# Kernel optimization log

Measured on AMD Instinct MI355X. Metric: run time of the kernel, lower is better.

## Reference

```python
import jax, jax.numpy as jnp
import numpy as np

EPS = 1e-5

def conv3x3(x, w, b):
    # x: [B,C,H,W], w: [O,I,3,3], padding=1 (SAME)
    y = jax.lax.conv_general_dilated(x, w, window_strides=(1, 1),
                                     padding=[(1, 1), (1, 1)],
                                     dimension_numbers=('NCHW', 'OIHW', 'NCHW'))
    return y + b[None, :, None, None]

def pool_block(x, k):
    # exact adaptive avg pool: 300 is divisible by the output size, block size k
    B, C, H, W = x.shape
    return x.reshape(B, C, H // k, k, W // k, k).mean(axis=(3, 5))

def upsample_nearest(x, k):
    # equivalent to the nested python-loop slice-assign in RIA
    return jnp.repeat(jnp.repeat(x, k, axis=2), k, axis=3)

def _conv_param(key, o, i):
    k1, k2 = jax.random.split(key)
    fan_in = i * 9
    w = jax.random.normal(k1, (o, i, 3, 3), jnp.float32) * np.sqrt(2.0 / fan_in)
    b = jax.random.normal(k2, (o,), jnp.float32) * 0.01
    return w, b

def setup_inputs() -> dict:
    key = jax.random.key(0)
    ks = jax.random.split(key, 16)
    inp = {}
    inp['im'] = jax.random.normal(ks[0], (32, 3, 300, 300), jnp.float32)
    inp['w1'], inp['b1'] = _conv_param(ks[1], 8, 3)
    inp['w2'], inp['b2'] = _conv_param(ks[2], 16, 8)
    inp['w3'], inp['b3'] = _conv_param(ks[3], 32, 16)
    inp['w4'], inp['b4'] = _conv_param(ks[4], 16, 32)
    inp['w5'], inp['b5'] = _conv_param(ks[5], 8, 16)
    inp['wc5'], inp['bc5'] = _conv_param(ks[6], 8, 16)
    inp['wc10'], inp['bc10'] = _conv_param(ks[7], 8, 16)
    inp['wc15'], inp['bc15'] = _conv_param(ks[8], 8, 16)
    inp['wg'], inp['bg'] = _conv_param(ks[9], 8, 24)
    inp['wm'], inp['bm'] = _conv_param(ks[10], 8, 24)
    inp['bn_w'] = jnp.ones((8,), jnp.float32)
    inp['bn_b'] = jnp.zeros((8,), jnp.float32)
    inp['w11'], inp['b11'] = _conv_param(ks[11], 1, 8)
    inp['gamma'] = jnp.full((1,), 0.3, jnp.float32)
    return inp

def reference(im, w1, b1, w2, b2, w3, b3, w4, b4, w5, b5,
              wc5, bc5, wc10, bc10, wc15, bc15,
              wg, bg, wm, bm, bn_w, bn_b, w11, b11, gamma):
    # attention conv chain 3->8->16->32->16->8
    x = conv3x3(im, w1, b1)
    x = conv3x3(x, w2, b2)
    x = conv3x3(x, w3, b3)
    x = conv3x3(x, w4, b4)
    x = conv3x3(x, w5, b5)  # [B,8,300,300]

    # RIA: triple-scale pooled context, nearest-upsampled and fused
    up5 = upsample_nearest(pool_block(x, 5), 5)
    up10 = upsample_nearest(pool_block(x, 10), 10)
    up15 = upsample_nearest(pool_block(x, 15), 15)
    c5 = conv3x3(jnp.concatenate([x, up5], axis=1), wc5, bc5)
    c10 = conv3x3(jnp.concatenate([x, up10], axis=1), wc10, bc10)
    c15 = conv3x3(jnp.concatenate([x, up15], axis=1), wc15, bc15)
    g_in = jnp.concatenate([c5, c10, c15], axis=1)  # [B,24,300,300]

    # gated conv (activation=None): conv(x) * sigmoid(mask_conv(x)), then BN (batch stats)
    gated = conv3x3(g_in, wg, bg) * jax.nn.sigmoid(conv3x3(g_in, wm, bm))
    mean = gated.mean(axis=(0, 2, 3), keepdims=True)
    var = gated.var(axis=(0, 2, 3), keepdims=True)
    gated = (gated - mean) * jax.lax.rsqrt(var + EPS)
    gated = gated * bn_w[None, :, None, None] + bn_b[None, :, None, None]

    # 8->1 conv, sigmoid attention map, residual gating with gamma
    att = jax.nn.sigmoid(conv3x3(gated, w11, b11))  # [B,1,300,300]
    out = gamma * (att * im) + (1.0 - gamma) * im
    return out
```

## Files before the change

kernel.cpp:

```cpp
#include <hip/hip_runtime.h>
#include <hip/hip_bf16.h>
#include <math.h>

typedef __hip_bfloat16 bf16;
typedef __attribute__((ext_vector_type(8))) __bf16 bf16x8;
typedef __attribute__((ext_vector_type(8))) unsigned short u16x8;
typedef __attribute__((ext_vector_type(4))) float f32x4;

#define H_ 300
#define W_ 300
#define HW_ 90000
#define NBATCH 32
#define RB 512

__device__ __forceinline__ float b2f(unsigned short u) {
    return __uint_as_float((unsigned int)u << 16);
}
__device__ __forceinline__ unsigned short f2u(float v) {
    bf16 b = __float2bfloat16(v);
    return *reinterpret_cast<unsigned short*>(&b);
}
__device__ __forceinline__ float sigm(float x) { return 1.f / (1.f + __expf(-x)); }
__device__ __forceinline__ unsigned int packbf(float a, float b) {
    return (unsigned int)f2u(a) | ((unsigned int)f2u(b) << 16);
}

__global__ void pack_all_k(
    const float* __restrict__ w1, const float* __restrict__ w2,
    const float* __restrict__ w3, const float* __restrict__ w4,
    const float* __restrict__ w5, const float* __restrict__ wc5,
    const float* __restrict__ wc10, const float* __restrict__ wc15,
    const float* __restrict__ wg, const float* __restrict__ wm,
    unsigned short* __restrict__ WP)
{
    const float *a = nullptr, *bsec = nullptr;
    int cs = 999, CO = 0, CI = 0, CP = 8, NS = 3, NG = 1, off = 0, special = 0;
    switch (blockIdx.x) {
        case 0: a = w2;  CO = 16; CI = 8;  CP = 8;  NS = 3; off = 0;     break;
        case 1: a = w3;  CO = 32; CI = 16; CP = 16; NS = 5; NG = 2; off = 2048;  break;
        case 2: a = w4;  CO = 16; CI = 32; CP = 32; NS = 9; off = 8192;  break;
        case 3: a = w5;  CO = 8;  CI = 16; CP = 16; NS = 5; off = 13312; break;
        case 4: special = 1; CO = 32; CI = 32; CP = 32; NS = 9; NG = 2;
                off = 16384; break;
        case 5: a = wg; bsec = wm; cs = 8; CO = 16; CI = 24; CP = 32; NS = 9;
                off = 25600; break;
        case 6: a = w1;  CO = 8;  CI = 3;  CP = 8;  NS = 3; off = 30720; break;
    }
    unsigned short* outp = WP + off;
    int TPK = 32 / CP;
    int total = NS * NG * 512;
    for (int idx = threadIdx.x; idx < total; idx += 256) {
        int j = idx & 7;
        int lane = (idx >> 3) & 63;
        int g = (idx >> 9) % NG;
        int s = idx / (512 * NG);
        int col = lane & 15, kg = lane >> 4;
        int kk = kg * 8 + j;
        int tt = kk / CP, ci = kk % CP;
        int tap = s * TPK + tt;
        float v = 0.f;
        if (special) {
            int o = ci >> 3, c8 = ci & 7;
            int convid = (g == 0) ? (col < 8 ? 0 : 1) : (col < 8 ? 2 : -1);
            if (tap < 9 && convid >= 0) {
                const float* wc = (convid == 0) ? wc5 : (convid == 1) ? wc10 : wc15;
                int colc = col & 7;
                if (o == 0) v = wc[(colc * 16 + c8) * 9 + tap];
                else if (o == convid + 1) v = wc[(colc * 16 + 8 + c8) * 9 + tap];
            }
        } else {
            int co = g * 16 + col;
            if (tap < 9 && ci < CI && co < CO)
                v = (co >= cs) ? bsec[((co - cs) * CI + ci) * 9 + tap]
                               : a[(co * CI + ci) * 9 + tap];
        }
        outp[idx] = f2u(v);
    }
}

template <int CIN, int CINP, int COUT, int NGI, int MODE, int TH>
__global__ __launch_bounds__(256) void mfconv_k(
    const unsigned short* __restrict__ src,
    const unsigned short* __restrict__ wpack,
    const float* __restrict__ bias0, const float* __restrict__ bias1,
    unsigned short* __restrict__ out, int co_total, int co_off)
{
    constexpr int TPK = 32 / CINP;
    constexpr int NSTEP = (9 + TPK - 1) / TPK;
    constexpr int OCT = CINP / 8;
    constexpr int NPX = (TH + 2) * 34;

    __shared__ __align__(16) unsigned short s_in[OCT * NPX * 8];

    int b = blockIdx.z;
    int x0 = blockIdx.x * 32, y0 = blockIdx.y * TH;
    int tid = threadIdx.x;
    int lane = tid & 63, wv = tid >> 6;
    bool interior = (x0 >= 1) && (x0 + 32 < W_) && (y0 >= 1) && (y0 + TH < H_);

    if (MODE == 3) {
        const float* sf = reinterpret_cast<const float*>(src) + (size_t)b * 3 * HW_;
        if (interior) {
            const float* sf0 = sf + (size_t)(y0 - 1) * W_ + (x0 - 1);
            for (int e = tid; e < NPX; e += 256) {
                int y = e / 34;
                size_t o = (size_t)e + (size_t)y * 266;
                u16x8 v = {0, 0, 0, 0, 0, 0, 0, 0};
                v[0] = f2u(sf0[o]);
                v[1] = f2u(sf0[HW_ + o]);
                v[2] = f2u(sf0[2 * HW_ + o]);
                *(u16x8*)&s_in[e * 8] = v;
            }
        } else {
            for (int e = tid; e < NPX; e += 256) {
                int y = e / 34, x = e - y * 34;
                int gy = y0 + y - 1, gx = x0 + x - 1;
                u16x8 v = {0, 0, 0, 0, 0, 0, 0, 0};
                if (gy >= 0 && gy < H_ && gx >= 0 && gx < W_) {
                    size_t o = (size_t)gy * W_ + gx;
                    v[0] = f2u(sf[o]);
                    v[1] = f2u(sf[HW_ + o]);
                    v[2] = f2u(sf[2 * HW_ + o]);
                }
                *(u16x8*)&s_in[e * 8] = v;
            }
        }
    } else {
        const unsigned short* sb = src + (size_t)b * CIN * HW_;
        int oct = (OCT == 1) ? 0 : (wv % OCT);
        int phase = (OCT == 4) ? 0 : (wv / OCT);
        if (interior) {
            const unsigned short* sb0 =
                sb + ((size_t)(y0 - 1) * W_ + (x0 - 1)) * CIN + oct * 8;
            for (int px = lane + phase * 64; px < NPX; px += 256 / OCT) {
                int y = px / 34;
                u16x8 v;
                if (CIN == CINP || oct * 8 < CIN)
                    v = *(const u16x8*)&sb0[(size_t)(px + y * 266) * CIN];
                else
                    v = (u16x8){0, 0, 0, 0, 0, 0, 0, 0};
                *(u16x8*)&s_in[(oct * NPX + px) * 8] = v;
            }
        } else {
            for (int px = lane + phase * 64; px < NPX; px += 256 / OCT) {
                int y = px / 34, x = px - y * 34;
                int gy = y0 + y - 1, gx = x0 + x - 1;
                u16x8 v = {0, 0, 0, 0, 0, 0, 0, 0};
                if (gy >= 0 && gy < H_ && gx >= 0 && gx < W_ &&
                    (CIN == CINP || oct * 8 < CIN))
                    v = *(const u16x8*)&sb[((size_t)gy * W_ + gx) * CIN + oct * 8];
                *(u16x8*)&s_in[(oct * NPX + px) * 8] = v;
            }
        }
    }

    bf16x8 bw[NGI][NSTEP];
#pragma unroll
    for (int gi = 0; gi < NGI; ++gi)
#pragma unroll
        for (int s = 0; s < NSTEP; ++s)
            bw[gi][s] = *(const bf16x8*)&wpack[((s * NGI + gi) * 64 + lane) * 8];

    int col = lane & 15, kg = lane >> 4;

    float bias_r[NGI][4];
#pragma unroll
    for (int gi = 0; gi < NGI; ++gi)
#pragma unroll
        for (int r = 0; r < 4; ++r) {
            if (MODE == 2)
                bias_r[0][r] = (kg < 2) ? bias0[kg * 4 + r] : bias1[(kg - 2) * 4 + r];
            else {
                int co_l = gi * 16 + kg * 4 + r;
                bias_r[gi][r] = (co_l < COUT) ? bias0[co_l] : 0.f;
            }
        }

    __syncthreads();

    if constexpr (OCT == 4) {
        int myb = wv * (TH / 4);
#pragma unroll
        for (int tx = 0; tx < 2; ++tx) {
            int pbase = kg * NPX + tx * 16 + col;
            bf16x8 fr[3][3];
#pragma unroll
            for (int r = 0; r < 2; ++r)
#pragma unroll
                for (int dx = 0; dx < 3; ++dx)
                    fr[r][dx] =
                        *(const bf16x8*)&s_in[(pbase + (myb + r) * 34 + dx) * 8];
#pragma unroll
            for (int ii = 0; ii < TH / 4; ++ii) {
#pragma unroll
                for (int dx = 0; dx < 3; ++dx)
                    fr[(ii + 2) % 3][dx] =
                        *(const bf16x8*)&s_in[(pbase + (myb + ii + 2) * 34 + dx) * 8];

                f32x4 acc[NGI];
#pragma unroll
                for (int gi = 0; gi < NGI; ++gi) acc[gi] = {0.f, 0.f, 0.f, 0.f};
#pragma unroll
                for (int dy = 0; dy < 3; ++dy)
#pragma unroll
                    for (int dx = 0; dx < 3; ++dx) {
                        bf16x8 a = fr[(ii + dy) % 3][dx];
#pragma unroll
                        for (int gi = 0; gi < NGI; ++gi)
                            acc[gi] = __builtin_amdgcn_mfma_f32_16x16x32_bf16(
                                bw[gi][dy * 3 + dx], a, acc[gi], 0, 0, 0);
                    }

                int gy = y0 + myb + ii;
                int gxx = x0 + tx * 16 + col;
                if (gy < H_) {
                    if (MODE == 2) {
                        float v0 = acc[0].x + bias_r[0][0];
                        float v1 = acc[0].y + bias_r[0][1];
                        float v2 = acc[0].z + bias_r[0][2];
                        float v3 = acc[0].w + bias_r[0][3];
                        float m0 = __shfl_xor(v0, 32), m1 = __shfl_xor(v1, 32);
                        float m2 = __shfl_xor(v2, 32), m3 = __shfl_xor(v3, 32);
                        if (kg < 2 && gxx < W_) {
                            uint2 st;
                            st.x = packbf(v0 * sigm(m0), v1 * sigm(m1));
                            st.y = packbf(v2 * sigm(m2), v3 * sigm(m3));
                            *(uint2*)&out[(((size_t)b * HW_ + (size_t)gy * W_ +
                                            gxx) * 8) + kg * 4] = st;
                        }
                    } else {
#pragma unroll
                        for (int gi = 0; gi < NGI; ++gi) {
                            int co_g = gi * 16 + kg * 4;
                            if (co_g < COUT && gxx < W_) {
                                uint2 st;
                                st.x = packbf(acc[gi].x + bias_r[gi][0],
                                              acc[gi].y + bias_r[gi][1]);
                                st.y = packbf(acc[gi].z + bias_r[gi][2],
                                              acc[gi].w + bias_r[gi][3]);
                                *(uint2*)&out[((size_t)b * HW_ +
                                               (size_t)gy * W_ + gxx) *
                                                  co_total + co_off + co_g] = st;
                            }
                        }
                    }
                }
            }
        }
    } else {
        int offs[NSTEP];
#pragma unroll
        for (int s = 0; s < NSTEP; ++s) {
            int t = s * TPK + kg / OCT;
            if (t > 8) t = 8;
            offs[s] = ((t / 3) * 34 + (t % 3)) * 8 + (kg % OCT) * (NPX * 8);
        }

#pragma unroll
        for (int i = 0; i < TH / 2; ++i) {
            int m = wv * (TH / 2) + i;
            int my = m >> 1, tx = m & 1;
            int gy = y0 + my;
            if (gy >= H_) continue;
            int base = (my * 34 + tx * 16 + col) * 8;

            f32x4 acc[NGI];
#pragma unroll
            for (int gi = 0; gi < NGI; ++gi) acc[gi] = {0.f, 0.f, 0.f, 0.f};
#pragma unroll
            for (int s = 0; s < NSTEP; ++s) {
                bf16x8 a = *(const bf16x8*)&s_in[base + offs[s]];
#pragma unroll
                for (int gi = 0; gi < NGI; ++gi)
                    acc[gi] = __builtin_amdgcn_mfma_f32_16x16x32_bf16(
                        bw[gi][s], a, acc[gi], 0, 0, 0);
            }

            int gxx = x0 + tx * 16 + col;
#pragma unroll
            for (int gi = 0; gi < NGI; ++gi) {
                int co_g = gi * 16 + kg * 4;
                if (co_g < COUT && gxx < W_) {
                    uint2 st;
                    st.x = packbf(acc[gi].x + bias_r[gi][0],
                                  acc[gi].y + bias_r[gi][1]);
                    st.y = packbf(acc[gi].z + bias_r[gi][2],
                                  acc[gi].w + bias_r[gi][3]);
                    *(uint2*)&out[((size_t)b * HW_ + (size_t)gy * W_ + gxx) *
                                      co_total + co_off + co_g] = st;
                }
            }
        }
    }
}

__global__ __launch_bounds__(256) void convc3_k(
    const unsigned short* __restrict__ src,
    const unsigned short* __restrict__ p5, const unsigned short* __restrict__ p10,
    const unsigned short* __restrict__ p15,
    const unsigned short* __restrict__ wpack,
    const float* __restrict__ bc5, const float* __restrict__ bc10,
    const float* __restrict__ bc15, unsigned short* __restrict__ out)
{
    constexpr int TH = 16;
    constexpr int NPX = (TH + 2) * 34;
    __shared__ __align__(16) unsigned short s_in[4 * NPX * 8];

    int b = blockIdx.z;
    int x0 = blockIdx.x * 32, y0 = blockIdx.y * TH;
    int tid = threadIdx.x;
    int lane = tid & 63, wv = tid >> 6;
    bool interior = (x0 >= 1) && (x0 + 32 < W_) && (y0 >= 1) && (y0 + TH < H_);

    const unsigned short* sb = src + (size_t)b * 8 * HW_;
    const unsigned short* pb5 = p5 + (size_t)b * 8 * 3600;
    const unsigned short* pb10 = p10 + (size_t)b * 8 * 900;
    const unsigned short* pb15 = p15 + (size_t)b * 8 * 400;

    int oct = wv;
    if (interior) {
        const unsigned short* sb0 = sb + ((size_t)(y0 - 1) * W_ + (x0 - 1)) * 8;
        for (int px = lane; px < NPX; px += 64) {
            int y = px / 34;
            u16x8 v;
            if (oct == 0) {
                v = *(const u16x8*)&sb0[(size_t)(px + y * 266) * 8];
            } else {
                int x = px - y * 34;
                int gy = y0 - 1 + y, gx = x0 - 1 + x;
                const unsigned short* pp =
                    (oct == 1) ? &pb5[((size_t)(gy / 5) * 60 + gx / 5) * 8]
                    : (oct == 2) ? &pb10[((size_t)(gy / 10) * 30 + gx / 10) * 8]
                                 : &pb15[((size_t)(gy / 15) * 20 + gx / 15) * 8];
                v = *(const u16x8*)pp;
            }
            *(u16x8*)&s_in[(oct * NPX + px) * 8] = v;
        }
    } else {
        for (int px = lane; px < NPX; px += 64) {
            int y = px / 34, x = px - y * 34;
            int gy = y0 + y - 1, gx = x0 + x - 1;
            u16x8 v = {0, 0, 0, 0, 0, 0, 0, 0};
            if (gy >= 0 && gy < H_ && gx >= 0 && gx < W_) {
                if (oct == 0)
                    v = *(const u16x8*)&sb[((size_t)gy * W_ + gx) * 8];
                else if (oct == 1)
                    v = *(const u16x8*)&pb5[((size_t)(gy / 5) * 60 + gx / 5) * 8];
                else if (oct == 2)
                    v = *(const u16x8*)&pb10[((size_t)(gy / 10) * 30 + gx / 10) * 8];
                else
                    v = *(const u16x8*)&pb15[((size_t)(gy / 15) * 20 + gx / 15) * 8];
            }
            *(u16x8*)&s_in[(oct * NPX + px) * 8] = v;
        }
    }

    bf16x8 bw[2][9];
#pragma unroll
    for (int g = 0; g < 2; ++g)
#pragma unroll
        for (int s = 0; s < 9; ++s)
            bw[g][s] = *(const bf16x8*)&wpack[((s * 2 + g) * 64 + lane) * 8];

    int col = lane & 15, kg = lane >> 4;
    float bias_r[2][4];
#pragma unroll
    for (int r = 0; r < 4; ++r) {
        bias_r[0][r] = (kg < 2) ? bc5[kg * 4 + r] : bc10[(kg - 2) * 4 + r];
        bias_r[1][r] = (kg < 2) ? bc15[kg * 4 + r] : 0.f;
    }

    __syncthreads();

    int myb = wv * (TH / 4);
#pragma unroll
    for (int tx = 0; tx < 2; ++tx) {
        int pbase = kg * NPX + tx * 16 + col;
        bf16x8 fr[3][3];
#pragma unroll
        for (int r = 0; r < 2; ++r)
#pragma unroll
            for (int dx = 0; dx < 3; ++dx)
                fr[r][dx] = *(const bf16x8*)&s_in[(pbase + (myb + r) * 34 + dx) * 8];
#pragma unroll
        for (int ii = 0; ii < TH / 4; ++ii) {
#pragma unroll
            for (int dx = 0; dx < 3; ++dx)
                fr[(ii + 2) % 3][dx] =
                    *(const bf16x8*)&s_in[(pbase + (myb + ii + 2) * 34 + dx) * 8];

            f32x4 acc[2];
            acc[0] = {0.f, 0.f, 0.f, 0.f};
            acc[1] = {0.f, 0.f, 0.f, 0.f};
#pragma unroll
            for (int dy = 0; dy < 3; ++dy)
#pragma unroll
                for (int dx = 0; dx < 3; ++dx) {
                    bf16x8 a = fr[(ii + dy) % 3][dx];
                    acc[0] = __builtin_amdgcn_mfma_f32_16x16x32_bf16(
                        bw[0][dy * 3 + dx], a, acc[0], 0, 0, 0);
                    acc[1] = __builtin_amdgcn_mfma_f32_16x16x32_bf16(
                        bw[1][dy * 3 + dx], a, acc[1], 0, 0, 0);
                }

            int gy = y0 + myb + ii;
            int gxx = x0 + tx * 16 + col;
            if (gy < H_ && gxx < W_) {
                size_t pxo = ((size_t)b * HW_ + (size_t)gy * W_ + gxx) * 24;
                uint2 st0;
                st0.x = packbf(acc[0].x + bias_r[0][0], acc[0].y + bias_r[0][1]);
                st0.y = packbf(acc[0].z + bias_r[0][2], acc[0].w + bias_r[0][3]);
                *(uint2*)&out[pxo + kg * 4] = st0;
                if (kg < 2) {
                    uint2 st1;
                    st1.x = packbf(acc[1].x + bias_r[1][0], acc[1].y + bias_r[1][1]);
                    st1.y = packbf(acc[1].z + bias_r[1][2], acc[1].w + bias_r[1][3]);
                    *(uint2*)&out[pxo + 16 + kg * 4] = st1;
                }
            }
        }
    }
}

__global__ __launch_bounds__(256) void pool5_k(const unsigned short* __restrict__ x,
                                               unsigned short* __restrict__ p5,
                                               int n)
{
    int idx = blockIdx.x * 256 + threadIdx.x;
    if (idx >= n) return;
    int b = idx / 3600;
    int rem = idx - b * 3600;
    int i = rem / 60, j = rem - i * 60;
    const unsigned short* src =
        x + ((size_t)b * HW_ + (size_t)(i * 5) * W_ + j * 5) * 8;
    float ss[8] = {0, 0, 0, 0, 0, 0, 0, 0};
#pragma unroll
    for (int r = 0; r < 5; ++r)
#pragma unroll
        for (int c = 0; c < 5; ++c) {
            u16x8 v = *(const u16x8*)&src[((size_t)r * W_ + c) * 8];
#pragma unroll
            for (int k = 0; k < 8; ++k) ss[k] += b2f(v[k]);
        }
    uint4 st;
    st.x = packbf(ss[0] * 0.04f, ss[1] * 0.04f);
    st.y = packbf(ss[2] * 0.04f, ss[3] * 0.04f);
    st.z = packbf(ss[4] * 0.04f, ss[5] * 0.04f);
    st.w = packbf(ss[6] * 0.04f, ss[7] * 0.04f);
    *(uint4*)&p5[(size_t)idx * 8] = st;
}

template <int R, int OD>
__device__ __forceinline__ void poolr_body(const unsigned short* __restrict__ p5,
                                           unsigned short* __restrict__ po, int idx)
{
    int b = idx / (OD * OD);
    int rem = idx - b * OD * OD;
    int i = rem / OD, j = rem - i * OD;
    const unsigned short* src =
        p5 + ((size_t)b * 3600 + (size_t)(i * R) * 60 + j * R) * 8;
    float ss[8] = {0, 0, 0, 0, 0, 0, 0, 0};
    const float inv = 1.f / (R * R);
#pragma unroll
    for (int r = 0; r < R; ++r)
#pragma unroll
        for (int c = 0; c < R; ++c) {
            u16x8 v = *(const u16x8*)&src[((size_t)r * 60 + c) * 8];
#pragma unroll
            for (int k = 0; k < 8; ++k) ss[k] += b2f(v[k]);
        }
    uint4 st;
    st.x = packbf(ss[0] * inv, ss[1] * inv);
    st.y = packbf(ss[2] * inv, ss[3] * inv);
    st.z = packbf(ss[4] * inv, ss[5] * inv);
    st.w = packbf(ss[6] * inv, ss[7] * inv);
    *(uint4*)&po[(size_t)idx * 8] = st;
}

__global__ __launch_bounds__(256) void poolrs_k(const unsigned short* __restrict__ p5,
                                                unsigned short* __restrict__ p10,
                                                unsigned short* __restrict__ p15,
                                                int n10, int n15)
{
    int idx = blockIdx.x * 256 + threadIdx.x;
    if (idx < n10) {
        poolr_body<2, 30>(p5, p10, idx);
    } else {
        idx -= n10;
        if (idx < n15) poolr_body<3, 20>(p5, p15, idx);
    }
}

__global__ __launch_bounds__(256) void reduce_k(
    const unsigned short* __restrict__ gated, float2* __restrict__ partials)
{
    int bx = blockIdx.x;
    int tid = threadIdx.x;
    float s[8] = {0, 0, 0, 0, 0, 0, 0, 0};
    float s2[8] = {0, 0, 0, 0, 0, 0, 0, 0};
    const size_t N = (size_t)NBATCH * HW_;
    for (size_t i = (size_t)bx * 256 + tid; i < N; i += (size_t)RB * 256) {
        u16x8 v = *(const u16x8*)&gated[i * 8];
#pragma unroll
        for (int k = 0; k < 8; ++k) {
            float f = b2f(v[k]);
            s[k] += f;
            s2[k] += f * f;
        }
    }
#pragma unroll
    for (int off = 32; off > 0; off >>= 1) {
#pragma unroll
        for (int k = 0; k < 8; ++k) {
            s[k] += __shfl_down(s[k], off);
            s2[k] += __shfl_down(s2[k], off);
        }
    }
    __shared__ float2 red[4][8];
    int lane = tid & 63, wvi = tid >> 6;
    if (lane == 0) {
#pragma unroll
        for (int k = 0; k < 8; ++k) red[wvi][k] = make_float2(s[k], s2[k]);
    }
    __syncthreads();
    if (tid < 8) {
        float a = 0.f, b2 = 0.f;
        for (int i = 0; i < 4; ++i) { a += red[i][tid].x; b2 += red[i][tid].y; }
        partials[tid * RB + bx] = make_float2(a, b2);
    }
}

__global__ __launch_bounds__(256) void stats_fold_k(
    const float2* __restrict__ partials, const float* __restrict__ bn_w,
    const float* __restrict__ bn_b, const float* __restrict__ w11,
    const float* __restrict__ b11, float* __restrict__ wfold)
{
    __shared__ float sc[8], tc[8];
    __shared__ float2 acc8[8];
    int tid = threadIdx.x;
    int c = tid >> 5, sl = tid & 31;
    float s = 0.f, s2 = 0.f;
    for (int i = sl; i < RB; i += 32) {
        float2 p = partials[c * RB + i];
        s += p.x;
        s2 += p.y;
    }
#pragma unroll
    for (int off = 16; off > 0; off >>= 1) {
        s += __shfl_down(s, off, 32);
        s2 += __shfl_down(s2, off, 32);
    }
    if (sl == 0) acc8[c] = make_float2(s, s2);
    __syncthreads();
    if (tid < 8) {
        double ds = acc8[tid].x, ds2 = acc8[tid].y;
        double N = (double)NBATCH * HW_;
        double mean = ds / N;
        double var = ds2 / N - mean * mean;
        float rstd = (float)(1.0 / sqrt(var + 1e-5));
        float scv = bn_w[tid] * rstd;
        sc[tid] = scv;
        tc[tid] = bn_b[tid] - (float)mean * scv;
    }
    __syncthreads();
    if (tid < 72) {
        int t = tid >> 3, ci = tid & 7;
        wfold[tid] = w11[ci * 9 + t] * sc[ci];
    }
    if (tid == 72) {
        float a = b11[0];
        for (int i = 0; i < 72; ++i) a += w11[i] * tc[i / 9];
        wfold[72] = a;
    }
}

__global__ __launch_bounds__(256) void final_k(
    const unsigned short* __restrict__ gated, const float* __restrict__ wf,
    const float* __restrict__ im, const float* __restrict__ gamma,
    float* __restrict__ out)
{
    __shared__ __align__(16) unsigned short s_g[1156 * 8];
    __shared__ float s_w[80];

    int b = blockIdx.z;
    int x0 = blockIdx.x * 32, y0 = blockIdx.y * 32;
    int tid = threadIdx.x;
    bool interior = (x0 >= 1) && (x0 + 32 < W_) && (y0 >= 1) && (y0 + 32 < H_);

    if (tid < 73) s_w[tid] = wf[tid];

    const unsigned short* gb = gated + (size_t)b * HW_ * 8;
    if (interior) {
        const unsigned short* gb0 = gb + ((size_t)(y0 - 1) * W_ + (x0 - 1)) * 8;
        for (int e = tid; e < 1156; e += 256) {
            int y = e / 34;
            u16x8 v = *(const u16x8*)&gb0[(size_t)(e + y * 266) * 8];
            *(u16x8*)&s_g[e * 8] = v;
        }
    } else {
        for (int e = tid; e < 1156; e += 256) {
            int y = e / 34, x = e - y * 34;
            int gy = y0 + y - 1, gx = x0 + x - 1;
            u16x8 v = {0, 0, 0, 0, 0, 0, 0, 0};
            if (gy >= 0 && gy < H_ && gx >= 0 && gx < W_)
                v = *(const u16x8*)&gb[((size_t)gy * W_ + gx) * 8];
            *(u16x8*)&s_g[e * 8] = v;
        }
    }
    __syncthreads();

    int qx = (tid & 15) * 2, qy = (tid >> 4) * 2;
    float f[4];
    float gm = *gamma;
#pragma unroll
    for (int p = 0; p < 4; ++p) {
        int ly = qy + (p >> 1), lx = qx + (p & 1);
        float acc = s_w[72];
#pragma unroll
        for (int t = 0; t < 9; ++t) {
            u16x8 n = *(const u16x8*)&s_g[((ly + t / 3) * 34 + lx + t % 3) * 8];
#pragma unroll
            for (int ci = 0; ci < 8; ++ci) acc += b2f(n[ci]) * s_w[t * 8 + ci];
        }
        f[p] = (1.f - gm) + gm * sigm(acc);
    }

    int px = x0 + qx, py = y0 + qy;
    if (px < W_) {
#pragma unroll
        for (int ch = 0; ch < 3; ++ch) {
            const float* imb = im + ((size_t)b * 3 + ch) * HW_;
            float* ob = out + ((size_t)b * 3 + ch) * HW_;
#pragma unroll
            for (int pr = 0; pr < 2; ++pr) {
                if (py + pr < H_) {
                    float2 iv = *(const float2*)&imb[(size_t)(py + pr) * W_ + px];
                    float2 ov;
                    ov.x = iv.x * f[pr * 2 + 0];
                    ov.y = iv.y * f[pr * 2 + 1];
                    *(float2*)&ob[(size_t)(py + pr) * W_ + px] = ov;
                }
            }
        }
    }
}


extern "C" void kernel_launch(void* const* d_in, const int* in_sizes, int n_in,
                              void* d_out, int out_size, void* d_ws,
                              size_t ws_size, hipStream_t stream)
{
    (void)in_sizes; (void)n_in; (void)out_size;

    const float* im  = (const float*)d_in[0];
    const float* w1  = (const float*)d_in[1];
    const float* b1  = (const float*)d_in[2];
    const float* w2  = (const float*)d_in[3];
    const float* b2  = (const float*)d_in[4];
    const float* w3  = (const float*)d_in[5];
    const float* b3  = (const float*)d_in[6];
    const float* w4  = (const float*)d_in[7];
    const float* b4  = (const float*)d_in[8];
    const float* w5  = (const float*)d_in[9];
    const float* b5  = (const float*)d_in[10];
    const float* wc5 = (const float*)d_in[11];
    const float* bc5 = (const float*)d_in[12];
    const float* wc10= (const float*)d_in[13];
    const float* bc10= (const float*)d_in[14];
    const float* wc15= (const float*)d_in[15];
    const float* bc15= (const float*)d_in[16];
    const float* wg  = (const float*)d_in[17];
    const float* bg  = (const float*)d_in[18];
    const float* wm  = (const float*)d_in[19];
    const float* bm  = (const float*)d_in[20];
    const float* bnw = (const float*)d_in[21];
    const float* bnb = (const float*)d_in[22];
    const float* w11 = (const float*)d_in[23];
    const float* b11 = (const float*)d_in[24];
    const float* gam = (const float*)d_in[25];
    float* out = (float*)d_out;

    const size_t GATED_B = 46080000;
    const size_t PER_IMG = 1440000 + 2880000 + 5760000 + 57600 + 14400 + 6656;
    const size_t MISC    = 262144;
    int c = 32;
    while (c > 1 && GATED_B + MISC + (size_t)c * PER_IMG + 2048 > ws_size)
        c >>= 1;

    char* p = (char*)d_ws;
    auto take = [&](size_t bytes) {
        char* r = p;
        p += (bytes + 255) & ~(size_t)255;
        return r;
    };
    unsigned short* GATED = (unsigned short*)take(GATED_B);
    unsigned short* A   = (unsigned short*)take((size_t)c * 1440000);
    unsigned short* Bb  = (unsigned short*)take((size_t)c * 2880000);
    unsigned short* C   = (unsigned short*)take((size_t)c * 5760000);
    unsigned short* P5  = (unsigned short*)take((size_t)c * 57600);
    unsigned short* P10 = (unsigned short*)take((size_t)c * 14400);
    unsigned short* P15 = (unsigned short*)take((size_t)c * 6656);
    float2* parts = (float2*)take(8 * RB * sizeof(float2));
    float*  wfold = (float*)take(512);
    unsigned short* WP = (unsigned short*)take(65536);

    unsigned short* PK2 = WP;
    unsigned short* PK3 = WP + 2048;
    unsigned short* PK4 = WP + 8192;
    unsigned short* PK5 = WP + 13312;
    unsigned short* PKc = WP + 16384;
    unsigned short* PKg = WP + 25600;
    unsigned short* PK1 = WP + 30720;

    dim3 blk(256);

    pack_all_k<<<dim3(7), blk, 0, stream>>>(w1, w2, w3, w4, w5, wc5, wc10, wc15,
                                            wg, wm, WP);

    for (int b0 = 0; b0 < NBATCH; b0 += c) {
        dim3 g32(10, 10, c);
        dim3 g16(10, 19, c);
        const float* imc = im + (size_t)b0 * 3 * HW_;

        mfconv_k<8, 8, 8, 1, 3, 32><<<g32, blk, 0, stream>>>(
            (const unsigned short*)imc, PK1, b1, nullptr, A, 8, 0);
        mfconv_k<8, 8, 16, 1, 0, 32><<<g32, blk, 0, stream>>>(
            A, PK2, b2, nullptr, Bb, 16, 0);
        mfconv_k<16, 16, 32, 2, 0, 32><<<g32, blk, 0, stream>>>(
            Bb, PK3, b3, nullptr, C, 32, 0);
        mfconv_k<32, 32, 16, 1, 0, 16><<<g16, blk, 0, stream>>>(
            C, PK4, b4, nullptr, Bb, 16, 0);
        mfconv_k<16, 16, 8, 1, 0, 32><<<g32, blk, 0, stream>>>(
            Bb, PK5, b5, nullptr, A, 8, 0);

        int n5 = c * 3600, n10 = c * 900, n15 = c * 400;
        pool5_k<<<dim3((n5 + 255) / 256), blk, 0, stream>>>(A, P5, n5);
        poolrs_k<<<dim3((n10 + n15 + 255) / 256), blk, 0, stream>>>(P5, P10, P15,
                                                                    n10, n15);

        convc3_k<<<g16, blk, 0, stream>>>(A, P5, P10, P15, PKc, bc5, bc10, bc15, C);

        mfconv_k<24, 32, 16, 1, 2, 16><<<g16, blk, 0, stream>>>(
            C, PKg, bg, bm, GATED + (size_t)b0 * HW_ * 8, 8, 0);
    }

    reduce_k<<<dim3(RB), blk, 0, stream>>>(GATED, parts);
    stats_fold_k<<<dim3(1), blk, 0, stream>>>(parts, bnw, bnb, w11, b11, wfold);
    final_k<<<dim3(10, 10, NBATCH), blk, 0, stream>>>(GATED, wfold, im, gam,
                                                      out);
}
```

Baseline: 463.6 us.

## Fuse batch-norm statistics into gated conv epilogue and merge pooling kernels

The gated conv kernel now accumulates per-channel sum and sum-of-squares of its fp32 outputs, reduces them within the block, and writes per-block partials. This removes the separate reduce pass that reread the whole bf16 gated tensor. The three pooling scales are merged into one kernel that pools directly from the full-resolution map instead of chaining off the 5x5 pool, trading extra reads for one fewer launch and dependency. bf16 packing now uses the v_cvt_pk_bf16_f32 instruction, and stats_fold has to sum many more partials.

```diff
diff --git a/kernel.cpp b/kernel.cpp
--- a/kernel.cpp
+++ b/kernel.cpp
@@ -11,7 +11,7 @@
 #define W_ 300
 #define HW_ 90000
 #define NBATCH 32
-#define RB 512
+#define NPART (NBATCH * 190)
 
 __device__ __forceinline__ float b2f(unsigned short u) {
     return __uint_as_float((unsigned int)u << 16);
@@ -22,7 +22,9 @@
 }
 __device__ __forceinline__ float sigm(float x) { return 1.f / (1.f + __expf(-x)); }
 __device__ __forceinline__ unsigned int packbf(float a, float b) {
-    return (unsigned int)f2u(a) | ((unsigned int)f2u(b) << 16);
+    unsigned int r;
+    asm("v_cvt_pk_bf16_f32 %0, %1, %2" : "=v"(r) : "v"(a), "v"(b));
+    return r;
 }
 
 __global__ void pack_all_k(
@@ -83,7 +85,8 @@
     const unsigned short* __restrict__ src,
     const unsigned short* __restrict__ wpack,
     const float* __restrict__ bias0, const float* __restrict__ bias1,
-    unsigned short* __restrict__ out, int co_total, int co_off)
+    unsigned short* __restrict__ out, int co_total, int co_off,
+    float2* __restrict__ bnp, int img_base)
 {
     constexpr int TPK = 32 / CINP;
     constexpr int NSTEP = (9 + TPK - 1) / TPK;
@@ -176,6 +179,8 @@
             }
         }
 
+    float bs[4] = {0.f, 0.f, 0.f, 0.f}, bs2[4] = {0.f, 0.f, 0.f, 0.f};
+
     __syncthreads();
 
     if constexpr (OCT == 4) {
@@ -222,11 +227,17 @@
                         float m0 = __shfl_xor(v0, 32), m1 = __shfl_xor(v1, 32);
                         float m2 = __shfl_xor(v2, 32), m3 = __shfl_xor(v3, 32);
                         if (kg < 2 && gxx < W_) {
+                            float o0 = v0 * sigm(m0), o1 = v1 * sigm(m1);
+                            float o2 = v2 * sigm(m2), o3 = v3 * sigm(m3);
                             uint2 st;
-                            st.x = packbf(v0 * sigm(m0), v1 * sigm(m1));
-                            st.y = packbf(v2 * sigm(m2), v3 * sigm(m3));
+                            st.x = packbf(o0, o1);
+                            st.y = packbf(o2, o3);
                             *(uint2*)&out[(((size_t)b * HW_ + (size_t)gy * W_ +
                                             gxx) * 8) + kg * 4] = st;
+                            bs[0] += o0; bs2[0] += o0 * o0;
+                            bs[1] += o1; bs2[1] += o1 * o1;
+                            bs[2] += o2; bs2[2] += o2 * o2;
+                            bs[3] += o3; bs2[3] += o3 * o3;
                         }
                     } else {
 #pragma unroll
@@ -290,6 +301,37 @@
                                       co_total + co_off + co_g] = st;
                 }
             }
+        }
+    }
+
+    if constexpr (MODE == 2) {
+#pragma unroll
+        for (int off = 1; off < 16; off <<= 1) {
+#pragma unroll
+            for (int r = 0; r < 4; ++r) {
+                bs[r] += __shfl_xor(bs[r], off);
+                bs2[r] += __shfl_xor(bs2[r], off);
+            }
+        }
+        __shared__ float bsum[4][8], bsq[4][8];
+        if (lane == 0) {
+#pragma unroll
+            for (int r = 0; r < 4; ++r) { bsum[wv][r] = bs[r]; bsq[wv][r] = bs2[r]; }
+        }
+        if (lane == 16) {
+#pragma unroll
+            for (int r = 0; r < 4; ++r) {
+                bsum[wv][4 + r] = bs[r];
+                bsq[wv][4 + r] = bs2[r];
+            }
+        }
+        __syncthreads();
+        if (tid < 8) {
+            float s = 0.f, s2 = 0.f;
+#pragma unroll
+            for (int w = 0; w < 4; ++w) { s += bsum[w][tid]; s2 += bsq[w][tid]; }
+            int bIdx = (img_base + b) * 190 + blockIdx.y * 10 + blockIdx.x;
+            bnp[(size_t)bIdx * 8 + tid] = make_float2(s, s2);
         }
     }
 }
@@ -422,50 +464,21 @@
     }
 }
 
-__global__ __launch_bounds__(256) void pool5_k(const unsigned short* __restrict__ x,
-                                               unsigned short* __restrict__ p5,
-                                               int n)
-{
-    int idx = blockIdx.x * 256 + threadIdx.x;
-    if (idx >= n) return;
-    int b = idx / 3600;
-    int rem = idx - b * 3600;
-    int i = rem / 60, j = rem - i * 60;
-    const unsigned short* src =
-        x + ((size_t)b * HW_ + (size_t)(i * 5) * W_ + j * 5) * 8;
-    float ss[8] = {0, 0, 0, 0, 0, 0, 0, 0};
-#pragma unroll
-    for (int r = 0; r < 5; ++r)
-#pragma unroll
-        for (int c = 0; c < 5; ++c) {
-            u16x8 v = *(const u16x8*)&src[((size_t)r * W_ + c) * 8];
-#pragma unroll
-            for (int k = 0; k < 8; ++k) ss[k] += b2f(v[k]);
-        }
-    uint4 st;
-    st.x = packbf(ss[0] * 0.04f, ss[1] * 0.04f);
-    st.y = packbf(ss[2] * 0.04f, ss[3] * 0.04f);
-    st.z = packbf(ss[4] * 0.04f, ss[5] * 0.04f);
-    st.w = packbf(ss[6] * 0.04f, ss[7] * 0.04f);
-    *(uint4*)&p5[(size_t)idx * 8] = st;
-}
-
-template <int R, int OD>
-__device__ __forceinline__ void poolr_body(const unsigned short* __restrict__ p5,
-                                           unsigned short* __restrict__ po, int idx)
+template <int K, int OD>
+__device__ __forceinline__ void pool_body(const unsigned short* __restrict__ x,
+                                          unsigned short* __restrict__ po, int idx)
 {
     int b = idx / (OD * OD);
     int rem = idx - b * OD * OD;
     int i = rem / OD, j = rem - i * OD;
     const unsigned short* src =
-        p5 + ((size_t)b * 3600 + (size_t)(i * R) * 60 + j * R) * 8;
+        x + ((size_t)b * HW_ + (size_t)(i * K) * W_ + j * K) * 8;
     float ss[8] = {0, 0, 0, 0, 0, 0, 0, 0};
-    const float inv = 1.f / (R * R);
-#pragma unroll
-    for (int r = 0; r < R; ++r)
-#pragma unroll
-        for (int c = 0; c < R; ++c) {
-            u16x8 v = *(const u16x8*)&src[((size_t)r * 60 + c) * 8];
+    const float inv = 1.f / (K * K);
+    for (int r = 0; r < K; ++r)
+#pragma unroll 5
+        for (int c = 0; c < K; ++c) {
+            u16x8 v = *(const u16x8*)&src[((size_t)r * W_ + c) * 8];
 #pragma unroll
             for (int k = 0; k < 8; ++k) ss[k] += b2f(v[k]);
         }
@@ -477,56 +490,18 @@
     *(uint4*)&po[(size_t)idx * 8] = st;
 }
 
-__global__ __launch_bounds__(256) void poolrs_k(const unsigned short* __restrict__ p5,
-                                                unsigned short* __restrict__ p10,
-                                                unsigned short* __restrict__ p15,
-                                                int n10, int n15)
+__global__ __launch_bounds__(256) void pools_k(
+    const unsigned short* __restrict__ x, unsigned short* __restrict__ p5,
+    unsigned short* __restrict__ p10, unsigned short* __restrict__ p15,
+    int n5, int n10, int n15)
 {
     int idx = blockIdx.x * 256 + threadIdx.x;
-    if (idx < n10) {
-        poolr_body<2, 30>(p5, p10, idx);
-    } else {
-        idx -= n10;
-        if (idx < n15) poolr_body<3, 20>(p5, p15, idx);
-    }
-}
-
-__global__ __launch_bounds__(256) void reduce_k(
-    const unsigned short* __restrict__ gated, float2* __restrict__ partials)
-{
-    int bx = blockIdx.x;
-    int tid = threadIdx.x;
-    float s[8] = {0, 0, 0, 0, 0, 0, 0, 0};
-    float s2[8] = {0, 0, 0, 0, 0, 0, 0, 0};
-    const size_t N = (size_t)NBATCH * HW_;
-    for (size_t i = (size_t)bx * 256 + tid; i < N; i += (size_t)RB * 256) {
-        u16x8 v = *(const u16x8*)&gated[i * 8];
-#pragma unroll
-        for (int k = 0; k < 8; ++k) {
-            float f = b2f(v[k]);
-            s[k] += f;
-            s2[k] += f * f;
-        }
-    }
-#pragma unroll
-    for (int off = 32; off > 0; off >>= 1) {
-#pragma unroll
-        for (int k = 0; k < 8; ++k) {
-            s[k] += __shfl_down(s[k], off);
-            s2[k] += __shfl_down(s2[k], off);
-        }
-    }
-    __shared__ float2 red[4][8];
-    int lane = tid & 63, wvi = tid >> 6;
-    if (lane == 0) {
-#pragma unroll
-        for (int k = 0; k < 8; ++k) red[wvi][k] = make_float2(s[k], s2[k]);
-    }
-    __syncthreads();
-    if (tid < 8) {
-        float a = 0.f, b2 = 0.f;
-        for (int i = 0; i < 4; ++i) { a += red[i][tid].x; b2 += red[i][tid].y; }
-        partials[tid * RB + bx] = make_float2(a, b2);
+    if (idx < n5) {
+        pool_body<5, 60>(x, p5, idx);
+    } else if (idx < n5 + n10) {
+        pool_body<10, 30>(x, p10, idx - n5);
+    } else if (idx < n5 + n10 + n15) {
+        pool_body<15, 20>(x, p15, idx - n5 - n10);
     }
 }
 
@@ -540,8 +515,8 @@
     int tid = threadIdx.x;
     int c = tid >> 5, sl = tid & 31;
     float s = 0.f, s2 = 0.f;
-    for (int i = sl; i < RB; i += 32) {
-        float2 p = partials[c * RB + i];
+    for (int i = sl; i < NPART; i += 32) {
+        float2 p = partials[(size_t)i * 8 + c];
         s += p.x;
         s2 += p.y;
     }
@@ -682,7 +657,7 @@
 
     const size_t GATED_B = 46080000;
     const size_t PER_IMG = 1440000 + 2880000 + 5760000 + 57600 + 14400 + 6656;
-    const size_t MISC    = 262144;
+    const size_t MISC    = 786432;
     int c = 32;
     while (c > 1 && GATED_B + MISC + (size_t)c * PER_IMG + 2048 > ws_size)
         c >>= 1;
@@ -700,7 +675,7 @@
     unsigned short* P5  = (unsigned short*)take((size_t)c * 57600);
     unsigned short* P10 = (unsigned short*)take((size_t)c * 14400);
     unsigned short* P15 = (unsigned short*)take((size_t)c * 6656);
-    float2* parts = (float2*)take(8 * RB * sizeof(float2));
+    float2* parts = (float2*)take((size_t)NPART * 8 * sizeof(float2));
     float*  wfold = (float*)take(512);
     unsigned short* WP = (unsigned short*)take(65536);
 
@@ -723,28 +698,26 @@
         const float* imc = im + (size_t)b0 * 3 * HW_;
 
         mfconv_k<8, 8, 8, 1, 3, 32><<<g32, blk, 0, stream>>>(
-            (const unsigned short*)imc, PK1, b1, nullptr, A, 8, 0);
+            (const unsigned short*)imc, PK1, b1, nullptr, A, 8, 0, nullptr, 0);
         mfconv_k<8, 8, 16, 1, 0, 32><<<g32, blk, 0, stream>>>(
-            A, PK2, b2, nullptr, Bb, 16, 0);
+            A, PK2, b2, nullptr, Bb, 16, 0, nullptr, 0);
         mfconv_k<16, 16, 32, 2, 0, 32><<<g32, blk, 0, stream>>>(
-            Bb, PK3, b3, nullptr, C, 32, 0);
+            Bb, PK3, b3, nullptr, C, 32, 0, nullptr, 0);
         mfconv_k<32, 32, 16, 1, 0, 16><<<g16, blk, 0, stream>>>(
-            C, PK4, b4, nullptr, Bb, 16, 0);
+            C, PK4, b4, nullptr, Bb, 16, 0, nullptr, 0);
         mfconv_k<16, 16, 8, 1, 0, 32><<<g32, blk, 0, stream>>>(
-            Bb, PK5, b5, nullptr, A, 8, 0);
+            Bb, PK5, b5, nullptr, A, 8, 0, nullptr, 0);
 
         int n5 = c * 3600, n10 = c * 900, n15 = c * 400;
-        pool5_k<<<dim3((n5 + 255) / 256), blk, 0, stream>>>(A, P5, n5);
-        poolrs_k<<<dim3((n10 + n15 + 255) / 256), blk, 0, stream>>>(P5, P10, P15,
-                                                                    n10, n15);
+        pools_k<<<dim3((n5 + n10 + n15 + 255) / 256), blk, 0, stream>>>(
+            A, P5, P10, P15, n5, n10, n15);
 
         convc3_k<<<g16, blk, 0, stream>>>(A, P5, P10, P15, PKc, bc5, bc10, bc15, C);
 
         mfconv_k<24, 32, 16, 1, 2, 16><<<g16, blk, 0, stream>>>(
-            C, PKg, bg, bm, GATED + (size_t)b0 * HW_ * 8, 8, 0);
-    }
-
-    reduce_k<<<dim3(RB), blk, 0, stream>>>(GATED, parts);
+            C, PKg, bg, bm, GATED + (size_t)b0 * HW_ * 8, 8, 0, parts, b0);
+    }
+
     stats_fold_k<<<dim3(1), blk, 0, stream>>>(parts, bnw, bnb, w11, b11, wfold);
     final_k<<<dim3(10, 10, NBATCH), blk, 0, stream>>>(GATED, wfold, im, gam,
                                                       out);
```

After: 544.2 us. 1.17x slower.
